# Optimization experiments

Hardware: AMD Instinct MI355X
Metric: run time of the kernel (lower is better)

## Reference

```python
import jax, jax.numpy as jnp
import numpy as np

N = 100000      # total nodes (10 graphs x 10000)
E = 1600000     # edges, avg degree 16
HN = 64         # hidden_node_dim
HE = 16         # hidden_edge_dim
IN_N, IN_E = 3, 1
L = 3           # conv_layers
B = 10          # num_graphs
NEG_SLOPE = 0.2
BN_EPS = 1e-5


def setup_inputs() -> dict:
    key = jax.random.key(0)
    ks = jax.random.split(key, 8)
    s = lambda d: 1.0 / np.sqrt(d)
    return {
        "x": jax.random.normal(ks[0], (N, IN_N), jnp.float32),
        "edge_attr": jax.random.uniform(ks[1], (E, IN_E), jnp.float32),
        "edge_index": jax.random.randint(ks[2], (2, E), 0, N, jnp.int64),
        "fc_node_w": jax.random.normal(ks[3], (IN_N, HN), jnp.float32) * s(IN_N),
        "fc_node_b": jnp.zeros((HN,), jnp.float32),
        "fc_edge_w": jax.random.normal(ks[4], (IN_E, HE), jnp.float32) * s(IN_E),
        "fc_edge_b": jnp.zeros((HE,), jnp.float32),
        "bn_gamma": jnp.ones((HN,), jnp.float32),
        "bn_beta": jnp.zeros((HN,), jnp.float32),
        "fc_w": jax.random.normal(ks[5], (L, HN, HN), jnp.float32) * s(HN),
        "fc_b": jnp.zeros((L, HN), jnp.float32),
        "attn_w": jax.random.normal(ks[6], (L, 2 * HN + HE, HN), jnp.float32) * s(2 * HN + HE),
        "attn_b": jnp.zeros((L, HN), jnp.float32),
        "batch_size": B,
    }


def segment_softmax(alpha, idx, num_segments):
    # PyG softmax: per-target-node, per-channel, numerically stable
    amax = jax.ops.segment_max(alpha, idx, num_segments=num_segments)
    amax = jnp.where(jnp.isfinite(amax), amax, 0.0)  # empty segments -> -inf
    ex = jnp.exp(alpha - amax[idx])
    denom = jax.ops.segment_sum(ex, idx, num_segments=num_segments)
    return ex / (denom[idx] + 1e-16)


def reference(x, edge_attr, edge_index, fc_node_w, fc_node_b, fc_edge_w, fc_edge_b,
              bn_gamma, bn_beta, fc_w, fc_b, attn_w, attn_b, batch_size):
    h = x @ fc_node_w + fc_node_b                 # [N, HN]
    e = edge_attr @ fc_edge_w + fc_edge_b        # [E, HE]
    # BatchNorm1d (training-mode batch statistics, biased variance)
    mean = jnp.mean(h, axis=0)
    var = jnp.mean((h - mean) ** 2, axis=0)
    h = (h - mean) * jax.lax.rsqrt(var + BN_EPS) * bn_gamma + bn_beta

    src, dst = edge_index[0], edge_index[1]      # x_j = h[src], x_i = h[dst]
    for l in range(L):
        hl = h @ fc_w[l] + fc_b[l]               # [N, HN]
        xi = hl[dst]                             # [E, HN]
        xj = hl[src]                             # [E, HN]
        cat = jnp.concatenate([xi, xj, e], axis=-1)  # [E, 2*HN+HE]
        alpha = cat @ attn_w[l] + attn_b[l]      # [E, HN]
        alpha = jax.nn.leaky_relu(alpha, NEG_SLOPE)
        alpha = segment_softmax(alpha, dst, N)
        h = jax.ops.segment_sum(xj * alpha, dst, num_segments=N)  # scatter-add aggregate
    return h.reshape(batch_size, -1, HN)
```

## Files before the change

kernel.cpp:

```cpp
#include <hip/hip_runtime.h>
#include <math.h>

#define NN 100000
#define NE 1600000
#define LAYERS 3
#define NEG 0.2f
#define BN_EPS 1e-5f

#define NB 196
#define NWG 128
#define CHUNK 12500
#define MOMB 304

typedef __attribute__((ext_vector_type(8))) short bf16x8;
typedef __attribute__((ext_vector_type(4))) float f32x4;

__device__ __forceinline__ unsigned f2bf(float x) {
    unsigned u = __float_as_uint(x);
    return (u + 0x7fffu + ((u >> 16) & 1u)) >> 16;
}

__global__ __launch_bounds__(256) void k_moments(const float* __restrict__ x,
    float* __restrict__ mom)
{
    float s0=0,s1=0,s2=0,m00=0,m01=0,m02=0,m11=0,m12=0,m22=0;
    for (int n = blockIdx.x * 256 + threadIdx.x; n < NN; n += MOMB * 256) {
        float a = x[n*3], b = x[n*3+1], c = x[n*3+2];
        s0 += a; s1 += b; s2 += c;
        m00 = fmaf(a,a,m00); m01 = fmaf(a,b,m01); m02 = fmaf(a,c,m02);
        m11 = fmaf(b,b,m11); m12 = fmaf(b,c,m12); m22 = fmaf(c,c,m22);
    }
    #pragma unroll
    for (int off = 32; off; off >>= 1) {
        s0 += __shfl_xor(s0, off); s1 += __shfl_xor(s1, off); s2 += __shfl_xor(s2, off);
        m00 += __shfl_xor(m00, off); m01 += __shfl_xor(m01, off); m02 += __shfl_xor(m02, off);
        m11 += __shfl_xor(m11, off); m12 += __shfl_xor(m12, off); m22 += __shfl_xor(m22, off);
    }
    __shared__ float red[4][9];
    int wave = threadIdx.x >> 6, lane = threadIdx.x & 63;
    if (lane == 0) {
        red[wave][0]=s0; red[wave][1]=s1; red[wave][2]=s2;
        red[wave][3]=m00; red[wave][4]=m01; red[wave][5]=m02;
        red[wave][6]=m11; red[wave][7]=m12; red[wave][8]=m22;
    }
    __syncthreads();
    if (threadIdx.x < 9) {
        float v = red[0][threadIdx.x] + red[1][threadIdx.x] + red[2][threadIdx.x] + red[3][threadIdx.x];
        atomicAdd(&mom[threadIdx.x], v);
    }
}

__global__ void k_params(const float* __restrict__ mom,
    const float* __restrict__ fnw, const float* __restrict__ fnb,
    const float* __restrict__ gamma, const float* __restrict__ beta,
    const float* __restrict__ few, const float* __restrict__ feb,
    const float* __restrict__ attn_w, const float* __restrict__ attn_b,
    const float* __restrict__ fcb, const float* __restrict__ fcw,
    float* __restrict__ bn_scale, float* __restrict__ u, float* __restrict__ c0,
    float* __restrict__ feff)
{
    __shared__ float ssh[64], sfe[3][64];
    int t = threadIdx.x;
    if (t < 64) {
        float w0 = fnw[t], w1 = fnw[64 + t], w2 = fnw[128 + t], bc = fnb[t];
        float dot  = mom[0]*w0 + mom[1]*w1 + mom[2]*w2;
        float quad = mom[3]*w0*w0 + 2.f*mom[4]*w0*w1 + 2.f*mom[5]*w0*w2
                   + mom[6]*w1*w1 + 2.f*mom[7]*w1*w2 + mom[8]*w2*w2;
        float mean = dot * (1.0f / NN) + bc;
        float eh2  = quad * (1.0f / NN) + 2.f * bc * dot * (1.0f / NN) + bc * bc;
        float var  = eh2 - mean * mean;
        float sc   = gamma[t] * rsqrtf(var + BN_EPS);
        bn_scale[t] = sc;
        ssh[t] = beta[t] - mean * sc;
    }
    __syncthreads();
    if (t < 64) {
        float v = 0.f;
        for (int k = 0; k < 64; k++) v = fmaf(ssh[k], fcw[k * 64 + t], v);
        sfe[0][t] = fcb[t] + v;
        sfe[1][t] = fcb[64 + t];
        sfe[2][t] = fcb[128 + t];
    }
    __syncthreads();
    if (t < 192) {
        int l = t >> 6, c = t & 63;
        const float* AW = attn_w + l * 144 * 64;
        float uu = 0.f, cc = 0.f;
        for (int j = 0; j < 16; j++) {
            float wv = AW[(128 + j) * 64 + c];
            uu = fmaf(few[j], wv, uu);
            cc = fmaf(feb[j], wv, cc);
        }
        float bi = 0.f;
        for (int tt = 0; tt < 64; tt++)
            bi = fmaf(sfe[l][tt], AW[tt * 64 + c] + AW[(64 + tt) * 64 + c], bi);
        u[t]    = uu;
        c0[t]   = cc + attn_b[t] + bi;
        feff[t] = sfe[l][c];
    }
}

__global__ __launch_bounds__(64) void k_prep(const float* __restrict__ fcw,
    const float* __restrict__ aw, const float* __restrict__ bscale,
    unsigned short* __restrict__ wt)
{
    int g = blockIdx.x, l = blockIdx.y, k = threadIdx.x;
    const float* W0 = fcw + l * 4096;
    float scale = (l == 0) ? bscale[k] : 1.0f;
    float v;
    if (g < 64) {
        v = W0[k * 64 + g] * scale;
    } else {
        int c = g & 63;
        const float* Wx = aw + l * 144 * 64 + (g < 128 ? 0 : 4096);
        float s = 0.f;
        for (int tt = 0; tt < 64; tt++) s = fmaf(W0[k * 64 + tt], Wx[tt * 64 + c], s);
        v = s * scale;
    }
    wt[(l * 192 + g) * 64 + k] = (unsigned short)f2bf(v);
}

__global__ __launch_bounds__(256) void k_bcount(const int* __restrict__ ei,
    int* __restrict__ counts)
{
    __shared__ int hist[NB];
    int t = threadIdx.x, wg = blockIdx.x;
    if (t < NB) hist[t] = 0;
    __syncthreads();
    int base = wg * CHUNK;
    for (int i = t; i < CHUNK; i += 256)
        atomicAdd(&hist[ei[NE + base + i] >> 9], 1);
    __syncthreads();
    if (t < NB) counts[t * NWG + wg] = hist[t];
}

__global__ __launch_bounds__(256) void k_bscan(int* __restrict__ counts,
    int* __restrict__ bbase, int* __restrict__ row_ptr)
{
    __shared__ int s_tot[256];
    int t = threadIdx.x;
    int tot = 0;
    if (t < NB)
        for (int w = 0; w < NWG; w++) tot += counts[t * NWG + w];
    s_tot[t] = tot;
    __syncthreads();
    for (int off = 1; off < 256; off <<= 1) {
        int v = (t >= off) ? s_tot[t - off] : 0;
        __syncthreads();
        s_tot[t] += v;
        __syncthreads();
    }
    int excl = s_tot[t] - tot;
    if (t < NB) {
        bbase[t] = excl;
        int run = excl;
        for (int w = 0; w < NWG; w++) {
            int c = counts[t * NWG + w];
            counts[t * NWG + w] = run;
            run += c;
        }
        if (t == NB - 1) {
            bbase[NB] = run;
            row_ptr[NN] = run;
        }
    }
}

__global__ __launch_bounds__(256) void k_bwrite(const int* __restrict__ ei,
    const float* __restrict__ ea, const int* __restrict__ counts,
    int2* __restrict__ brec)
{
    __shared__ int off[NB];
    int t = threadIdx.x, wg = blockIdx.x;
    if (t < NB) off[t] = counts[t * NWG + wg];
    __syncthreads();
    int base = wg * CHUNK;
    for (int i = t; i < CHUNK; i += 256) {
        int k = base + i;
        int s = ei[k], d = ei[NE + k];
        int b = d >> 9;
        int j = atomicAdd(&off[b], 1);
        brec[j] = make_int2(((d & 511) << 17) | s, __float_as_int(ea[k]));
    }
}

__global__ __launch_bounds__(256) void k_csr(const int2* __restrict__ brec,
    const int* __restrict__ bbase, int* __restrict__ row_ptr, int2* __restrict__ er)
{
    __shared__ int s_cnt[512], s_excl[512], s_ts[256];
    int t = threadIdx.x, b = blockIdx.x;
    int beg = bbase[b], end = bbase[b + 1];
    s_cnt[t] = 0; s_cnt[t + 256] = 0;
    __syncthreads();
    for (int i = beg + t; i < end; i += 256)
        atomicAdd(&s_cnt[brec[i].x >> 17], 1);
    __syncthreads();
    int a0 = s_cnt[2 * t], a1 = s_cnt[2 * t + 1];
    int ts = a0 + a1;
    s_ts[t] = ts;
    __syncthreads();
    for (int off = 1; off < 256; off <<= 1) {
        int v = (t >= off) ? s_ts[t - off] : 0;
        __syncthreads();
        s_ts[t] += v;
        __syncthreads();
    }
    int et = s_ts[t] - ts;
    s_excl[2 * t] = et; s_excl[2 * t + 1] = et + a0;
    s_cnt[t] = 0; s_cnt[t + 256] = 0;
    __syncthreads();
    #pragma unroll
    for (int q = 0; q < 2; q++) {
        int dl = t + q * 256;
        int n = b * 512 + dl;
        if (n < NN) row_ptr[n] = beg + s_excl[dl];
    }
    for (int i = beg + t; i < end; i += 256) {
        int2 r = brec[i];
        int dl = r.x >> 17;
        int pos = atomicAdd(&s_cnt[dl], 1);
        er[beg + s_excl[dl] + pos] = make_int2(r.x & 0x1FFFF, r.y);
    }
}

template<bool FIRST>
__global__ __launch_bounds__(256) void k_tf(const float* __restrict__ h,
    const float* __restrict__ xin, const float* __restrict__ fnw, const float* __restrict__ fnb,
    const unsigned short* __restrict__ wt_l, const float* __restrict__ feff_l,
    float* __restrict__ ai, unsigned* __restrict__ packed)
{
    int tid = threadIdx.x;
    int wv = tid >> 6, l = tid & 63;
    int r16 = l & 15, quad = l >> 4;
    int n0 = blockIdx.x * 64 + wv * 16;
    int na = n0 + r16; if (na >= NN) na = NN - 1;
    bf16x8 a[2];
    if (FIRST) {
        float x0 = xin[na*3], x1 = xin[na*3+1], x2 = xin[na*3+2];
        #pragma unroll
        for (int ks = 0; ks < 2; ks++) {
            bf16x8 t;
            #pragma unroll
            for (int e = 0; e < 8; e++) {
                int c = quad * 8 + ks * 32 + e;
                float v = fmaf(x0, fnw[c], fmaf(x1, fnw[64 + c], fmaf(x2, fnw[128 + c], fnb[c])));
                t[e] = (short)f2bf(v);
            }
            a[ks] = t;
        }
    } else {
        const float* hp = h + (size_t)na * 64 + quad * 8;
        #pragma unroll
        for (int ks = 0; ks < 2; ks++) {
            f32x4 lo = *(const f32x4*)(hp + ks * 32);
            f32x4 hi = *(const f32x4*)(hp + ks * 32 + 4);
            bf16x8 t;
            t[0] = (short)f2bf(lo[0]); t[1] = (short)f2bf(lo[1]);
            t[2] = (short)f2bf(lo[2]); t[3] = (short)f2bf(lo[3]);
            t[4] = (short)f2bf(hi[0]); t[5] = (short)f2bf(hi[1]);
            t[6] = (short)f2bf(hi[2]); t[7] = (short)f2bf(hi[3]);
            a[ks] = t;
        }
    }
    f32x4 acc[12];
    #pragma unroll
    for (int i = 0; i < 12; i++) acc[i] = (f32x4){0.f, 0.f, 0.f, 0.f};
    const unsigned short* wb = wt_l + (size_t)r16 * 64 + quad * 8;
    #pragma unroll
    for (int cb = 0; cb < 12; cb++) {
        bf16x8 b0 = *(const bf16x8*)(wb + cb * 1024);
        bf16x8 b1 = *(const bf16x8*)(wb + cb * 1024 + 32);
        acc[cb] = __builtin_amdgcn_mfma_f32_16x16x32_bf16(a[0], b0, acc[cb], 0, 0, 0);
        acc[cb] = __builtin_amdgcn_mfma_f32_16x16x32_bf16(a[1], b1, acc[cb], 0, 0, 0);
    }
    #pragma unroll
    for (int r = 0; r < 4; r++) {
        int nd = n0 + quad * 4 + r;
        if (nd < NN) {
            size_t base = (size_t)nd * 64 + r16;
            #pragma unroll
            for (int cq = 0; cq < 4; cq++) {
                float hlv = acc[cq][r] + feff_l[cq * 16 + r16];
                float aiv = acc[4 + cq][r];
                float ajv = acc[8 + cq][r];
                ai[base + cq * 16]     = aiv;
                packed[base + cq * 16] = f2bf(hlv) | (f2bf(ajv) << 16);
            }
        }
    }
}

__global__ __launch_bounds__(256) void k_edge(const unsigned* __restrict__ packed,
    const float* __restrict__ ai, const int* __restrict__ row_ptr,
    const int2* __restrict__ er, const float* __restrict__ u, const float* __restrict__ c0,
    float* __restrict__ hout, int l)
{
    int w = threadIdx.x >> 6, c = threadIdx.x & 63;
    int n = blockIdx.x * 4 + w;
    int beg = row_ptr[n], end = row_ptr[n + 1];
    float base = ai[n * 64 + c] + c0[l * 64 + c];
    float uc = u[l * 64 + c];
    const unsigned* __restrict__ pc = packed + c;
    float d0 = 0.f, d1 = 0.f, s0 = 0.f, s1 = 0.f;
    int k = beg;
    for (; k + 8 <= end; k += 8) {
        int2 e[8]; unsigned p[8];
        #pragma unroll
        for (int q = 0; q < 8; q++) e[q] = er[k + q];
        #pragma unroll
        for (int q = 0; q < 8; q++) p[q] = pc[(size_t)e[q].x << 6];
        #pragma unroll
        for (int q = 0; q < 8; q++) {
            float a = fmaf(__int_as_float(e[q].y), uc, base + __uint_as_float(p[q] & 0xffff0000u));
            a = fmaxf(a, NEG * a);
            float xx = __expf(a);
            if (q & 1) { d1 += xx; s1 = fmaf(xx, __uint_as_float(p[q] << 16), s1); }
            else       { d0 += xx; s0 = fmaf(xx, __uint_as_float(p[q] << 16), s0); }
        }
    }
    for (; k + 4 <= end; k += 4) {
        int2 e[4]; unsigned p[4];
        #pragma unroll
        for (int q = 0; q < 4; q++) e[q] = er[k + q];
        #pragma unroll
        for (int q = 0; q < 4; q++) p[q] = pc[(size_t)e[q].x << 6];
        #pragma unroll
        for (int q = 0; q < 4; q++) {
            float a = fmaf(__int_as_float(e[q].y), uc, base + __uint_as_float(p[q] & 0xffff0000u));
            a = fmaxf(a, NEG * a);
            float xx = __expf(a);
            if (q & 1) { d1 += xx; s1 = fmaf(xx, __uint_as_float(p[q] << 16), s1); }
            else       { d0 += xx; s0 = fmaf(xx, __uint_as_float(p[q] << 16), s0); }
        }
    }
    for (; k < end; k++) {
        int2 e0 = er[k];
        unsigned p0 = pc[(size_t)e0.x << 6];
        float a0 = fmaf(__int_as_float(e0.y), uc, base + __uint_as_float(p0 & 0xffff0000u));
        a0 = fmaxf(a0, NEG * a0);
        float x0 = __expf(a0);
        d0 += x0;
        s0 = fmaf(x0, __uint_as_float(p0 << 16), s0);
    }
    hout[n * 64 + c] = (s0 + s1) / (d0 + d1 + 1e-16f);
}

extern "C" void kernel_launch(void* const* d_in, const int* in_sizes, int n_in,
                              void* d_out, int out_size, void* d_ws, size_t ws_size,
                              hipStream_t stream)
{
    const float* x    = (const float*)d_in[0];
    const float* ea   = (const float*)d_in[1];
    const int*   ei   = (const int*)d_in[2];
    const float* fnw  = (const float*)d_in[3];
    const float* fnb  = (const float*)d_in[4];
    const float* few  = (const float*)d_in[5];
    const float* feb  = (const float*)d_in[6];
    const float* gmm  = (const float*)d_in[7];
    const float* beta = (const float*)d_in[8];
    const float* fcw  = (const float*)d_in[9];
    const float* fcb  = (const float*)d_in[10];
    const float* aw   = (const float*)d_in[11];
    const float* ab   = (const float*)d_in[12];
    float* out = (float*)d_out;

    char* ws = (char*)d_ws;
    size_t off = 0;
    auto alloc = [&](size_t bytes) -> void* {
        void* p = ws + off;
        off += (bytes + 255) / 256 * 256;
        return p;
    };
    float*    h       = (float*)   alloc((size_t)NN * 64 * 4);
    float*    ai      = (float*)   alloc((size_t)NN * 64 * 4);
    unsigned* packed  = (unsigned*)alloc((size_t)NN * 64 * 4);
    int2*     er      = (int2*)    alloc((size_t)NE * 8);
    int2*     brec    = (int2*)    alloc((size_t)NE * 8);
    int*      row_ptr = (int*)     alloc((size_t)(NN + 1) * 4);
    int*      counts  = (int*)     alloc((size_t)NB * NWG * 4);
    int*      bbase   = (int*)     alloc((NB + 1) * 4);
    float*    mom     = (float*)   alloc(12 * 4);
    float*    bscale  = (float*)   alloc(64 * 4);
    float*    uvec    = (float*)   alloc(192 * 4);
    float*    c0vec   = (float*)   alloc(192 * 4);
    float*    feff    = (float*)   alloc(192 * 4);
    unsigned short* wt = (unsigned short*)alloc((size_t)LAYERS * 192 * 64 * 2);

    hipMemsetAsync(mom, 0, 12 * 4, stream);

    k_moments<<<MOMB, 256, 0, stream>>>(x, mom);
    k_params<<<1, 256, 0, stream>>>(mom, fnw, fnb, gmm, beta, few, feb, aw, ab, fcb, fcw,
                                    bscale, uvec, c0vec, feff);
    k_prep<<<dim3(192, LAYERS), 64, 0, stream>>>(fcw, aw, bscale, wt);

    k_bcount<<<NWG, 256, 0, stream>>>(ei, counts);
    k_bscan<<<1, 256, 0, stream>>>(counts, bbase, row_ptr);
    k_bwrite<<<NWG, 256, 0, stream>>>(ei, ea, counts, brec);
    k_csr<<<NB, 256, 0, stream>>>(brec, bbase, row_ptr, er);

    for (int l = 0; l < LAYERS; l++) {
        if (l == 0)
            k_tf<true><<<(NN + 63) / 64, 256, 0, stream>>>(h, x, fnw, fnb,
                wt, feff, ai, packed);
        else
            k_tf<false><<<(NN + 63) / 64, 256, 0, stream>>>(h, x, fnw, fnb,
                wt + (size_t)l * 192 * 64, feff + l * 64, ai, packed);
        float* ho = (l == LAYERS - 1) ? out : h;
        k_edge<<<NN / 4, 256, 0, stream>>>(packed, ai, row_ptr, er,
                                           uvec, c0vec, ho, l);
    }
    (void)in_sizes; (void)n_in; (void)out_size; (void)ws_size;
}
```

Measured before the change: 489.8 us.

## Merge independent setup kernels into combined launches to cut launch count

Independent preprocessing stages are packed into the same grids, with blocks branching on blockIdx. Edge bucket counting now runs alongside the input moments, and the scan runs with the parameter and weight-prep work. The first-layer transform runs in the same grid as the bucket write. The c0 bias is folded into the stored ai so the edge kernel reads one fewer vector. This aims to remove per-launch overhead and serial gaps between small kernels, but the block-role dispatch makes load balance inside each grid less even.

After: 460.7 us. 5.9% less time.

```diff
diff --git a/kernel.cpp b/kernel.cpp
--- a/kernel.cpp
+++ b/kernel.cpp
@@ -11,6 +11,7 @@
 #define NWG 128
 #define CHUNK 12500
 #define MOMB 304
+#define TFB 1563
 
 typedef __attribute__((ext_vector_type(8))) short bf16x8;
 typedef __attribute__((ext_vector_type(4))) float f32x4;
@@ -20,167 +21,232 @@
     return (u + 0x7fffu + ((u >> 16) & 1u)) >> 16;
 }
 
-__global__ __launch_bounds__(256) void k_moments(const float* __restrict__ x,
-    float* __restrict__ mom)
-{
-    float s0=0,s1=0,s2=0,m00=0,m01=0,m02=0,m11=0,m12=0,m22=0;
-    for (int n = blockIdx.x * 256 + threadIdx.x; n < NN; n += MOMB * 256) {
-        float a = x[n*3], b = x[n*3+1], c = x[n*3+2];
-        s0 += a; s1 += b; s2 += c;
-        m00 = fmaf(a,a,m00); m01 = fmaf(a,b,m01); m02 = fmaf(a,c,m02);
-        m11 = fmaf(b,b,m11); m12 = fmaf(b,c,m12); m22 = fmaf(c,c,m22);
-    }
-    #pragma unroll
-    for (int off = 32; off; off >>= 1) {
-        s0 += __shfl_xor(s0, off); s1 += __shfl_xor(s1, off); s2 += __shfl_xor(s2, off);
-        m00 += __shfl_xor(m00, off); m01 += __shfl_xor(m01, off); m02 += __shfl_xor(m02, off);
-        m11 += __shfl_xor(m11, off); m12 += __shfl_xor(m12, off); m22 += __shfl_xor(m22, off);
-    }
-    __shared__ float red[4][9];
-    int wave = threadIdx.x >> 6, lane = threadIdx.x & 63;
-    if (lane == 0) {
-        red[wave][0]=s0; red[wave][1]=s1; red[wave][2]=s2;
-        red[wave][3]=m00; red[wave][4]=m01; red[wave][5]=m02;
-        red[wave][6]=m11; red[wave][7]=m12; red[wave][8]=m22;
-    }
-    __syncthreads();
-    if (threadIdx.x < 9) {
-        float v = red[0][threadIdx.x] + red[1][threadIdx.x] + red[2][threadIdx.x] + red[3][threadIdx.x];
-        atomicAdd(&mom[threadIdx.x], v);
-    }
-}
-
-__global__ void k_params(const float* __restrict__ mom,
+__global__ __launch_bounds__(256) void k_front(const int* __restrict__ ei,
+    int* __restrict__ counts, const float* __restrict__ x, float* __restrict__ mom)
+{
+    int t = threadIdx.x;
+    if (blockIdx.x < NWG) {
+        __shared__ int hist[NB];
+        int wg = blockIdx.x;
+        if (t < NB) hist[t] = 0;
+        __syncthreads();
+        int base = wg * CHUNK;
+        for (int i = t; i < CHUNK; i += 256)
+            atomicAdd(&hist[ei[NE + base + i] >> 9], 1);
+        __syncthreads();
+        if (t < NB) counts[t * NWG + wg] = hist[t];
+    } else {
+        int mb = blockIdx.x - NWG;
+        float s0=0,s1=0,s2=0,m00=0,m01=0,m02=0,m11=0,m12=0,m22=0;
+        for (int n = mb * 256 + t; n < NN; n += MOMB * 256) {
+            float a = x[n*3], b = x[n*3+1], c = x[n*3+2];
+            s0 += a; s1 += b; s2 += c;
+            m00 = fmaf(a,a,m00); m01 = fmaf(a,b,m01); m02 = fmaf(a,c,m02);
+            m11 = fmaf(b,b,m11); m12 = fmaf(b,c,m12); m22 = fmaf(c,c,m22);
+        }
+        #pragma unroll
+        for (int off = 32; off; off >>= 1) {
+            s0 += __shfl_xor(s0, off); s1 += __shfl_xor(s1, off); s2 += __shfl_xor(s2, off);
+            m00 += __shfl_xor(m00, off); m01 += __shfl_xor(m01, off); m02 += __shfl_xor(m02, off);
+            m11 += __shfl_xor(m11, off); m12 += __shfl_xor(m12, off); m22 += __shfl_xor(m22, off);
+        }
+        __shared__ float red[4][9];
+        int wave = t >> 6, lane = t & 63;
+        if (lane == 0) {
+            red[wave][0]=s0; red[wave][1]=s1; red[wave][2]=s2;
+            red[wave][3]=m00; red[wave][4]=m01; red[wave][5]=m02;
+            red[wave][6]=m11; red[wave][7]=m12; red[wave][8]=m22;
+        }
+        __syncthreads();
+        if (t < 9) {
+            float v = red[0][t] + red[1][t] + red[2][t] + red[3][t];
+            atomicAdd(&mom[t], v);
+        }
+    }
+}
+
+__device__ __forceinline__ float bn_scale_of(const float* __restrict__ mom,
+    const float* __restrict__ fnw, const float* __restrict__ fnb,
+    const float* __restrict__ gamma, int k)
+{
+    float w0 = fnw[k], w1 = fnw[64 + k], w2 = fnw[128 + k], bc = fnb[k];
+    float dot  = mom[0]*w0 + mom[1]*w1 + mom[2]*w2;
+    float quad = mom[3]*w0*w0 + 2.f*mom[4]*w0*w1 + 2.f*mom[5]*w0*w2
+               + mom[6]*w1*w1 + 2.f*mom[7]*w1*w2 + mom[8]*w2*w2;
+    float mean = dot * (1.0f / NN) + bc;
+    float eh2  = quad * (1.0f / NN) + 2.f * bc * dot * (1.0f / NN) + bc * bc;
+    float var  = eh2 - mean * mean;
+    return gamma[k] * rsqrtf(var + BN_EPS);
+}
+
+__global__ __launch_bounds__(256) void k_mid(const float* __restrict__ mom,
     const float* __restrict__ fnw, const float* __restrict__ fnb,
     const float* __restrict__ gamma, const float* __restrict__ beta,
     const float* __restrict__ few, const float* __restrict__ feb,
     const float* __restrict__ attn_w, const float* __restrict__ attn_b,
     const float* __restrict__ fcb, const float* __restrict__ fcw,
-    float* __restrict__ bn_scale, float* __restrict__ u, float* __restrict__ c0,
-    float* __restrict__ feff)
-{
-    __shared__ float ssh[64], sfe[3][64];
+    int* __restrict__ counts, int* __restrict__ bbase, int* __restrict__ row_ptr,
+    float* __restrict__ u, float* __restrict__ c0, float* __restrict__ feff,
+    unsigned short* __restrict__ wt)
+{
     int t = threadIdx.x;
-    if (t < 64) {
-        float w0 = fnw[t], w1 = fnw[64 + t], w2 = fnw[128 + t], bc = fnb[t];
-        float dot  = mom[0]*w0 + mom[1]*w1 + mom[2]*w2;
-        float quad = mom[3]*w0*w0 + 2.f*mom[4]*w0*w1 + 2.f*mom[5]*w0*w2
-                   + mom[6]*w1*w1 + 2.f*mom[7]*w1*w2 + mom[8]*w2*w2;
-        float mean = dot * (1.0f / NN) + bc;
-        float eh2  = quad * (1.0f / NN) + 2.f * bc * dot * (1.0f / NN) + bc * bc;
-        float var  = eh2 - mean * mean;
-        float sc   = gamma[t] * rsqrtf(var + BN_EPS);
-        bn_scale[t] = sc;
-        ssh[t] = beta[t] - mean * sc;
-    }
-    __syncthreads();
-    if (t < 64) {
-        float v = 0.f;
-        for (int k = 0; k < 64; k++) v = fmaf(ssh[k], fcw[k * 64 + t], v);
-        sfe[0][t] = fcb[t] + v;
-        sfe[1][t] = fcb[64 + t];
-        sfe[2][t] = fcb[128 + t];
-    }
-    __syncthreads();
-    if (t < 192) {
-        int l = t >> 6, c = t & 63;
-        const float* AW = attn_w + l * 144 * 64;
-        float uu = 0.f, cc = 0.f;
-        for (int j = 0; j < 16; j++) {
-            float wv = AW[(128 + j) * 64 + c];
-            uu = fmaf(few[j], wv, uu);
-            cc = fmaf(feb[j], wv, cc);
-        }
-        float bi = 0.f;
-        for (int tt = 0; tt < 64; tt++)
-            bi = fmaf(sfe[l][tt], AW[tt * 64 + c] + AW[(64 + tt) * 64 + c], bi);
-        u[t]    = uu;
-        c0[t]   = cc + attn_b[t] + bi;
-        feff[t] = sfe[l][c];
-    }
-}
-
-__global__ __launch_bounds__(64) void k_prep(const float* __restrict__ fcw,
-    const float* __restrict__ aw, const float* __restrict__ bscale,
-    unsigned short* __restrict__ wt)
-{
-    int g = blockIdx.x, l = blockIdx.y, k = threadIdx.x;
-    const float* W0 = fcw + l * 4096;
-    float scale = (l == 0) ? bscale[k] : 1.0f;
-    float v;
-    if (g < 64) {
-        v = W0[k * 64 + g] * scale;
+    if (blockIdx.x == 0) {
+        __shared__ float ssh[64], sfe[3][64];
+        if (t < 64) {
+            float w0 = fnw[t], w1 = fnw[64 + t], w2 = fnw[128 + t], bc = fnb[t];
+            float dot  = mom[0]*w0 + mom[1]*w1 + mom[2]*w2;
+            float quad = mom[3]*w0*w0 + 2.f*mom[4]*w0*w1 + 2.f*mom[5]*w0*w2
+                       + mom[6]*w1*w1 + 2.f*mom[7]*w1*w2 + mom[8]*w2*w2;
+            float mean = dot * (1.0f / NN) + bc;
+            float eh2  = quad * (1.0f / NN) + 2.f * bc * dot * (1.0f / NN) + bc * bc;
+            float var  = eh2 - mean * mean;
+            float sc   = gamma[t] * rsqrtf(var + BN_EPS);
+            ssh[t] = beta[t] - mean * sc;
+        }
+        __syncthreads();
+        if (t < 64) {
+            float v = 0.f;
+            for (int k = 0; k < 64; k++) v = fmaf(ssh[k], fcw[k * 64 + t], v);
+            sfe[0][t] = fcb[t] + v;
+            sfe[1][t] = fcb[64 + t];
+            sfe[2][t] = fcb[128 + t];
+        }
+        __syncthreads();
+        if (t < 192) {
+            int l = t >> 6, c = t & 63;
+            const float* AW = attn_w + l * 144 * 64;
+            float uu = 0.f, cc = 0.f;
+            for (int j = 0; j < 16; j++) {
+                float wv = AW[(128 + j) * 64 + c];
+                uu = fmaf(few[j], wv, uu);
+                cc = fmaf(feb[j], wv, cc);
+            }
+            float bi = 0.f;
+            for (int tt = 0; tt < 64; tt++)
+                bi = fmaf(sfe[l][tt], AW[tt * 64 + c] + AW[(64 + tt) * 64 + c], bi);
+            u[t]    = uu;
+            c0[t]   = cc + attn_b[t] + bi;
+            feff[t] = sfe[l][c];
+        }
+    } else if (blockIdx.x == 1) {
+        __shared__ int s_tot[256];
+        int tot = 0;
+        if (t < NB)
+            for (int w = 0; w < NWG; w++) tot += counts[t * NWG + w];
+        s_tot[t] = tot;
+        __syncthreads();
+        for (int off = 1; off < 256; off <<= 1) {
+            int v = (t >= off) ? s_tot[t - off] : 0;
+            __syncthreads();
+            s_tot[t] += v;
+            __syncthreads();
+        }
+        int excl = s_tot[t] - tot;
+        if (t < NB) {
+            bbase[t] = excl;
+            int run = excl;
+            for (int w = 0; w < NWG; w++) {
+                int c = counts[t * NWG + w];
+                counts[t * NWG + w] = run;
+                run += c;
+            }
+            if (t == NB - 1) {
+                bbase[NB] = run;
+                row_ptr[NN] = run;
+            }
+        }
     } else {
-        int c = g & 63;
-        const float* Wx = aw + l * 144 * 64 + (g < 128 ? 0 : 4096);
-        float s = 0.f;
-        for (int tt = 0; tt < 64; tt++) s = fmaf(W0[k * 64 + tt], Wx[tt * 64 + c], s);
-        v = s * scale;
-    }
-    wt[(l * 192 + g) * 64 + k] = (unsigned short)f2bf(v);
-}
-
-__global__ __launch_bounds__(256) void k_bcount(const int* __restrict__ ei,
-    int* __restrict__ counts)
-{
-    __shared__ int hist[NB];
-    int t = threadIdx.x, wg = blockIdx.x;
-    if (t < NB) hist[t] = 0;
-    __syncthreads();
-    int base = wg * CHUNK;
-    for (int i = t; i < CHUNK; i += 256)
-        atomicAdd(&hist[ei[NE + base + i] >> 9], 1);
-    __syncthreads();
-    if (t < NB) counts[t * NWG + wg] = hist[t];
-}
-
-__global__ __launch_bounds__(256) void k_bscan(int* __restrict__ counts,
-    int* __restrict__ bbase, int* __restrict__ row_ptr)
-{
-    __shared__ int s_tot[256];
+        int task = (blockIdx.x - 2) * 4 + (t >> 6);
+        int k = t & 63;
+        int l = task / 192, g = task - l * 192;
+        const float* W0 = fcw + l * 4096;
+        float scale = (l == 0) ? bn_scale_of(mom, fnw, fnb, gamma, k) : 1.0f;
+        float v;
+        if (g < 64) {
+            v = W0[k * 64 + g] * scale;
+        } else {
+            int c = g & 63;
+            const float* Wx = attn_w + l * 144 * 64 + (g < 128 ? 0 : 4096);
+            float s = 0.f;
+            for (int tt = 0; tt < 64; tt++) s = fmaf(W0[k * 64 + tt], Wx[tt * 64 + c], s);
+            v = s * scale;
+        }
+        wt[(l * 192 + g) * 64 + k] = (unsigned short)f2bf(v);
+    }
+}
+
+__device__ __forceinline__ void tf_core(const bf16x8* a, const unsigned short* __restrict__ wt_l,
+    const float* __restrict__ feff_l, const float* __restrict__ c0_l,
+    float* __restrict__ ai, unsigned* __restrict__ packed, int n0, int r16, int quad)
+{
+    f32x4 acc[12];
+    #pragma unroll
+    for (int i = 0; i < 12; i++) acc[i] = (f32x4){0.f, 0.f, 0.f, 0.f};
+    const unsigned short* wb = wt_l + (size_t)r16 * 64 + quad * 8;
+    #pragma unroll
+    for (int cb = 0; cb < 12; cb++) {
+        bf16x8 b0 = *(const bf16x8*)(wb + cb * 1024);
+        bf16x8 b1 = *(const bf16x8*)(wb + cb * 1024 + 32);
+        acc[cb] = __builtin_amdgcn_mfma_f32_16x16x32_bf16(a[0], b0, acc[cb], 0, 0, 0);
+        acc[cb] = __builtin_amdgcn_mfma_f32_16x16x32_bf16(a[1], b1, acc[cb], 0, 0, 0);
+    }
+    #pragma unroll
+    for (int r = 0; r < 4; r++) {
+        int nd = n0 + quad * 4 + r;
+        if (nd < NN) {
+            size_t base = (size_t)nd * 64 + r16;
+            #pragma unroll
+            for (int cq = 0; cq < 4; cq++) {
+                float hlv = acc[cq][r] + feff_l[cq * 16 + r16];
+                float aiv = acc[4 + cq][r] + c0_l[cq * 16 + r16];
+                float ajv = acc[8 + cq][r];
+                ai[base + cq * 16]     = aiv;
+                packed[base + cq * 16] = f2bf(hlv) | (f2bf(ajv) << 16);
+            }
+        }
+    }
+}
+
+__global__ __launch_bounds__(256) void k_l3(const int* __restrict__ ei,
+    const float* __restrict__ ea, const int* __restrict__ counts, int2* __restrict__ brec,
+    const float* __restrict__ xin, const float* __restrict__ fnw, const float* __restrict__ fnb,
+    const unsigned short* __restrict__ wt, const float* __restrict__ feff,
+    const float* __restrict__ c0v, float* __restrict__ ai, unsigned* __restrict__ packed)
+{
     int t = threadIdx.x;
-    int tot = 0;
-    if (t < NB)
-        for (int w = 0; w < NWG; w++) tot += counts[t * NWG + w];
-    s_tot[t] = tot;
-    __syncthreads();
-    for (int off = 1; off < 256; off <<= 1) {
-        int v = (t >= off) ? s_tot[t - off] : 0;
-        __syncthreads();
-        s_tot[t] += v;
-        __syncthreads();
-    }
-    int excl = s_tot[t] - tot;
-    if (t < NB) {
-        bbase[t] = excl;
-        int run = excl;
-        for (int w = 0; w < NWG; w++) {
-            int c = counts[t * NWG + w];
-            counts[t * NWG + w] = run;
-            run += c;
-        }
-        if (t == NB - 1) {
-            bbase[NB] = run;
-            row_ptr[NN] = run;
-        }
-    }
-}
-
-__global__ __launch_bounds__(256) void k_bwrite(const int* __restrict__ ei,
-    const float* __restrict__ ea, const int* __restrict__ counts,
-    int2* __restrict__ brec)
-{
-    __shared__ int off[NB];
-    int t = threadIdx.x, wg = blockIdx.x;
-    if (t < NB) off[t] = counts[t * NWG + wg];
-    __syncthreads();
-    int base = wg * CHUNK;
-    for (int i = t; i < CHUNK; i += 256) {
-        int k = base + i;
-        int s = ei[k], d = ei[NE + k];
-        int b = d >> 9;
-        int j = atomicAdd(&off[b], 1);
-        brec[j] = make_int2(((d & 511) << 17) | s, __float_as_int(ea[k]));
+    if (blockIdx.x < NWG) {
+        __shared__ int off[NB];
+        int wg = blockIdx.x;
+        if (t < NB) off[t] = counts[t * NWG + wg];
+        __syncthreads();
+        int base = wg * CHUNK;
+        for (int i = t; i < CHUNK; i += 256) {
+            int k = base + i;
+            int s = ei[k], d = ei[NE + k];
+            int b = d >> 9;
+            int j = atomicAdd(&off[b], 1);
+            brec[j] = make_int2(((d & 511) << 17) | s, __float_as_int(ea[k]));
+        }
+    } else {
+        int bid = blockIdx.x - NWG;
+        int wv = t >> 6, l = t & 63;
+        int r16 = l & 15, quad = l >> 4;
+        int n0 = bid * 64 + wv * 16;
+        int na = n0 + r16; if (na >= NN) na = NN - 1;
+        float x0 = xin[na*3], x1 = xin[na*3+1], x2 = xin[na*3+2];
+        bf16x8 a[2];
+        #pragma unroll
+        for (int ks = 0; ks < 2; ks++) {
+            bf16x8 tt;
+            #pragma unroll
+            for (int e = 0; e < 8; e++) {
+                int c = quad * 8 + ks * 32 + e;
+                float v = fmaf(x0, fnw[c], fmaf(x1, fnw[64 + c], fmaf(x2, fnw[128 + c], fnb[c])));
+                tt[e] = (short)f2bf(v);
+            }
+            a[ks] = tt;
+        }
+        tf_core(a, wt, feff, c0v, ai, packed, n0, r16, quad);
     }
 }
 
@@ -223,83 +289,41 @@
     }
 }
 
-template<bool FIRST>
 __global__ __launch_bounds__(256) void k_tf(const float* __restrict__ h,
-    const float* __restrict__ xin, const float* __restrict__ fnw, const float* __restrict__ fnb,
     const unsigned short* __restrict__ wt_l, const float* __restrict__ feff_l,
-    float* __restrict__ ai, unsigned* __restrict__ packed)
-{
-    int tid = threadIdx.x;
-    int wv = tid >> 6, l = tid & 63;
+    const float* __restrict__ c0_l, float* __restrict__ ai, unsigned* __restrict__ packed)
+{
+    int t = threadIdx.x;
+    int wv = t >> 6, l = t & 63;
     int r16 = l & 15, quad = l >> 4;
     int n0 = blockIdx.x * 64 + wv * 16;
     int na = n0 + r16; if (na >= NN) na = NN - 1;
+    const float* hp = h + (size_t)na * 64 + quad * 8;
     bf16x8 a[2];
-    if (FIRST) {
-        float x0 = xin[na*3], x1 = xin[na*3+1], x2 = xin[na*3+2];
-        #pragma unroll
-        for (int ks = 0; ks < 2; ks++) {
-            bf16x8 t;
-            #pragma unroll
-            for (int e = 0; e < 8; e++) {
-                int c = quad * 8 + ks * 32 + e;
-                float v = fmaf(x0, fnw[c], fmaf(x1, fnw[64 + c], fmaf(x2, fnw[128 + c], fnb[c])));
-                t[e] = (short)f2bf(v);
-            }
-            a[ks] = t;
-        }
-    } else {
-        const float* hp = h + (size_t)na * 64 + quad * 8;
-        #pragma unroll
-        for (int ks = 0; ks < 2; ks++) {
-            f32x4 lo = *(const f32x4*)(hp + ks * 32);
-            f32x4 hi = *(const f32x4*)(hp + ks * 32 + 4);
-            bf16x8 t;
-            t[0] = (short)f2bf(lo[0]); t[1] = (short)f2bf(lo[1]);
-            t[2] = (short)f2bf(lo[2]); t[3] = (short)f2bf(lo[3]);
-            t[4] = (short)f2bf(hi[0]); t[5] = (short)f2bf(hi[1]);
-            t[6] = (short)f2bf(hi[2]); t[7] = (short)f2bf(hi[3]);
-            a[ks] = t;
-        }
-    }
-    f32x4 acc[12];
     #pragma unroll
-    for (int i = 0; i < 12; i++) acc[i] = (f32x4){0.f, 0.f, 0.f, 0.f};
-    const unsigned short* wb = wt_l + (size_t)r16 * 64 + quad * 8;
-    #pragma unroll
-    for (int cb = 0; cb < 12; cb++) {
-        bf16x8 b0 = *(const bf16x8*)(wb + cb * 1024);
-        bf16x8 b1 = *(const bf16x8*)(wb + cb * 1024 + 32);
-        acc[cb] = __builtin_amdgcn_mfma_f32_16x16x32_bf16(a[0], b0, acc[cb], 0, 0, 0);
-        acc[cb] = __builtin_amdgcn_mfma_f32_16x16x32_bf16(a[1], b1, acc[cb], 0, 0, 0);
-    }
-    #pragma unroll
-    for (int r = 0; r < 4; r++) {
-        int nd = n0 + quad * 4 + r;
-        if (nd < NN) {
-            size_t base = (size_t)nd * 64 + r16;
-            #pragma unroll
-            for (int cq = 0; cq < 4; cq++) {
-                float hlv = acc[cq][r] + feff_l[cq * 16 + r16];
-                float aiv = acc[4 + cq][r];
-                float ajv = acc[8 + cq][r];
-                ai[base + cq * 16]     = aiv;
-                packed[base + cq * 16] = f2bf(hlv) | (f2bf(ajv) << 16);
-            }
-        }
-    }
+    for (int ks = 0; ks < 2; ks++) {
+        f32x4 lo = *(const f32x4*)(hp + ks * 32);
+        f32x4 hi = *(const f32x4*)(hp + ks * 32 + 4);
+        bf16x8 tt;
+        tt[0] = (short)f2bf(lo[0]); tt[1] = (short)f2bf(lo[1]);
+        tt[2] = (short)f2bf(lo[2]); tt[3] = (short)f2bf(lo[3]);
+        tt[4] = (short)f2bf(hi[0]); tt[5] = (short)f2bf(hi[1]);
+        tt[6] = (short)f2bf(hi[2]); tt[7] = (short)f2bf(hi[3]);
+        a[ks] = tt;
+    }
+    tf_core(a, wt_l, feff_l, c0_l, ai, packed, n0, r16, quad);
 }
 
 __global__ __launch_bounds__(256) void k_edge(const unsigned* __restrict__ packed,
     const float* __restrict__ ai, const int* __restrict__ row_ptr,
-    const int2* __restrict__ er, const float* __restrict__ u, const float* __restrict__ c0,
-    float* __restrict__ hout, int l)
+    const int2* __restrict__ er, const float* __restrict__ u_l,
+    float* __restrict__ hout)
 {
     int w = threadIdx.x >> 6, c = threadIdx.x & 63;
     int n = blockIdx.x * 4 + w;
     int beg = row_ptr[n], end = row_ptr[n + 1];
-    float base = ai[n * 64 + c] + c0[l * 64 + c];
-    float uc = u[l * 64 + c];
+    float base = ai[n * 64 + c];
+    float uc = u_l[c];
     const unsigned* __restrict__ pc = packed + c;
     float d0 = 0.f, d1 = 0.f, s0 = 0.f, s1 = 0.f;
     int k = beg;
@@ -380,34 +404,24 @@
     int*      counts  = (int*)     alloc((size_t)NB * NWG * 4);
     int*      bbase   = (int*)     alloc((NB + 1) * 4);
     float*    mom     = (float*)   alloc(12 * 4);
-    float*    bscale  = (float*)   alloc(64 * 4);
     float*    uvec    = (float*)   alloc(192 * 4);
     float*    c0vec   = (float*)   alloc(192 * 4);
     float*    feff    = (float*)   alloc(192 * 4);
     unsigned short* wt = (unsigned short*)alloc((size_t)LAYERS * 192 * 64 * 2);
 
-    hipMemsetAsync(mom, 0, 12 * 4, stream);
-
-    k_moments<<<MOMB, 256, 0, stream>>>(x, mom);
-    k_params<<<1, 256, 0, stream>>>(mom, fnw, fnb, gmm, beta, few, feb, aw, ab, fcb, fcw,
-                                    bscale, uvec, c0vec, feff);
-    k_prep<<<dim3(192, LAYERS), 64, 0, stream>>>(fcw, aw, bscale, wt);
-
-    k_bcount<<<NWG, 256, 0, stream>>>(ei, counts);
-    k_bscan<<<1, 256, 0, stream>>>(counts, bbase, row_ptr);
-    k_bwrite<<<NWG, 256, 0, stream>>>(ei, ea, counts, brec);
+    (void)hipMemsetAsync(mom, 0, 12 * 4, stream);
+
+    k_front<<<NWG + MOMB, 256, 0, stream>>>(ei, counts, x, mom);
+    k_mid<<<2 + 144, 256, 0, stream>>>(mom, fnw, fnb, gmm, beta, few, feb, aw, ab,
+                                       fcb, fcw, counts, bbase, row_ptr,
+                                       uvec, c0vec, feff, wt);
+    k_l3<<<NWG + TFB, 256, 0, stream>>>(ei, ea, counts, brec, x, fnw, fnb,
+                                        wt, feff, c0vec, ai, packed);
     k_csr<<<NB, 256, 0, stream>>>(brec, bbase, row_ptr, er);
-
-    for (int l = 0; l < LAYERS; l++) {
-        if (l == 0)
-            k_tf<true><<<(NN + 63) / 64, 256, 0, stream>>>(h, x, fnw, fnb,
-                wt, feff, ai, packed);
-        else
-            k_tf<false><<<(NN + 63) / 64, 256, 0, stream>>>(h, x, fnw, fnb,
-                wt + (size_t)l * 192 * 64, feff + l * 64, ai, packed);
-        float* ho = (l == LAYERS - 1) ? out : h;
-        k_edge<<<NN / 4, 256, 0, stream>>>(packed, ai, row_ptr, er,
-                                           uvec, c0vec, ho, l);
-    }
+    k_edge<<<NN / 4, 256, 0, stream>>>(packed, ai, row_ptr, er, uvec, h);
+    k_tf<<<TFB, 256, 0, stream>>>(h, wt + (size_t)192 * 64, feff + 64, c0vec + 64, ai, packed);
+    k_edge<<<NN / 4, 256, 0, stream>>>(packed, ai, row_ptr, er, uvec + 64, h);
+    k_tf<<<TFB, 256, 0, stream>>>(h, wt + (size_t)2 * 192 * 64, feff + 128, c0vec + 128, ai, packed);
+    k_edge<<<NN / 4, 256, 0, stream>>>(packed, ai, row_ptr, er, uvec + 128, out);
     (void)in_sizes; (void)n_in; (void)out_size; (void)ws_size;
 }
```
